# Kernel optimization log

Hardware: AMD Instinct MI355X
Metric: run time of the kernel (lower is better)

## Reference

```python
import jax, jax.numpy as jnp
import numpy as np

B, H, L, V = 128, 1024, 60, 50257


def setup_inputs() -> dict:
    key = jax.random.key(0)
    ks = jax.random.split(key, 14)
    s = 0.02
    f32 = jnp.float32
    return {
        "input": jax.random.randint(ks[0], (B,), 0, V),
        "hidden": jax.random.normal(ks[1], (1, B, H), f32),
        "encoder_outputs": jax.random.normal(ks[2], (B, L, H), f32),
        # learned parameters
        "emb": (jax.random.normal(ks[3], (V, H), f32) * s),
        "attn_W": (jax.random.normal(ks[4], (L, 2 * H), f32) * s),
        "attn_b": jnp.zeros((L,), f32),
        "comb_W": (jax.random.normal(ks[5], (H, 2 * H), f32) * s),
        "comb_b": jnp.zeros((H,), f32),
        "W_ih": (jax.random.normal(ks[6], (3 * H, H), f32) * s),
        "W_hh": (jax.random.normal(ks[7], (3 * H, H), f32) * s),
        "b_ih": jnp.zeros((3 * H,), f32),
        "b_hh": jnp.zeros((3 * H,), f32),
        "out_W": (jax.random.normal(ks[8], (V, H), f32) * s),
        "out_b": jnp.zeros((V,), f32),
    }


def reference(input, hidden, encoder_outputs, emb, attn_W, attn_b,
              comb_W, comb_b, W_ih, W_hh, b_ih, b_hh, out_W, out_b):
    # embedding lookup (dropout is identity in eval mode)
    embedded = emb[input]                      # [B, H]
    h = hidden[0]                              # [B, H]

    # Bahdanau-style attention over fixed max_length positions
    attn_logits = jnp.concatenate([embedded, h], axis=1) @ attn_W.T + attn_b  # [B, L]
    attn_weights = jax.nn.softmax(attn_logits, axis=1)                        # [B, L]
    attn_applied = jnp.einsum('bl,blh->bh', attn_weights, encoder_outputs)    # [B, H]

    # combine + relu
    x = jnp.concatenate([embedded, attn_applied], axis=1) @ comb_W.T + comb_b  # [B, H]
    x = jax.nn.relu(x)

    # single GRU step (PyTorch gate order: r, z, n)
    gi = x @ W_ih.T + b_ih                     # [B, 3H]
    gh = h @ W_hh.T + b_hh                     # [B, 3H]
    i_r, i_z, i_n = jnp.split(gi, 3, axis=1)
    h_r, h_z, h_n = jnp.split(gh, 3, axis=1)
    r = jax.nn.sigmoid(i_r + h_r)
    z = jax.nn.sigmoid(i_z + h_z)
    n = jnp.tanh(i_n + r * h_n)
    h_new = (1.0 - z) * n + z * h              # [B, H]

    # output projection + log_softmax over vocab
    logp = jax.nn.log_softmax(h_new @ out_W.T + out_b, axis=1)  # [B, V]
    return logp, h_new[None], attn_weights
```

## Files before the change

### kernel.cpp

```cpp
#include <hip/hip_runtime.h>
#include <hip/hip_bf16.h>

#define B_ 128
#define H_ 1024
#define L_ 60
#define V_ 50257

typedef __attribute__((ext_vector_type(8))) short bf16x8;
typedef __attribute__((ext_vector_type(4))) short bf16x4;
typedef __attribute__((ext_vector_type(4))) float f32x4;

__device__ __forceinline__ unsigned short f2bf(float f) {
  union { __hip_bfloat16 h; unsigned short u; } v;
  v.h = __float2bfloat16(f);
  return v.u;
}

__device__ __forceinline__ void gl_lds16(const void* g, void* l) {
  __builtin_amdgcn_global_load_lds(
      (const __attribute__((address_space(1))) unsigned int*)g,
      (__attribute__((address_space(3))) unsigned int*)l, 16, 0, 0);
}

#define SBAR()   __builtin_amdgcn_s_barrier()
#define SCHED0() __builtin_amdgcn_sched_barrier(0)
__device__ __forceinline__ void lwait0() { asm volatile("s_waitcnt lgkmcnt(0)" ::: "memory"); }
__device__ __forceinline__ void vwait4() { asm volatile("s_waitcnt vmcnt(4)" ::: "memory"); }
__device__ __forceinline__ void vwait0() { asm volatile("s_waitcnt vmcnt(0)" ::: "memory"); }

__device__ __forceinline__ size_t packIdx(int b, int k) {
  int s = k >> 5;
  int bm = b >> 4;
  int lane = (b & 15) | (((k >> 3) & 3) << 4);
  return ((size_t)((s * 8 + bm) * 64 + lane) << 3) | (size_t)(k & 7);
}

__global__ __launch_bounds__(256) void k_front(
    const int* __restrict__ input, const float* __restrict__ hidden,
    const float* __restrict__ emb, const float* __restrict__ attn_W,
    const float* __restrict__ attn_b, unsigned short* __restrict__ aXa,
    unsigned short* __restrict__ aH, float* __restrict__ lbuf)
{
  int bx = blockIdx.x;
  if (bx < 512) {
    int idx = bx * 256 + threadIdx.x;
    int b = idx >> 10, j = idx & (H_ - 1);
    float e = emb[(size_t)input[b] * H_ + j];
    float h = hidden[idx];
    size_t p = packIdx(b, j);
    aXa[p] = f2bf(e);
    aH[p]  = f2bf(h);
  } else {
    int t = threadIdx.x, wv = t >> 6, lane = t & 63;
    int task = (bx - 512) * 4 + wv;
    int b = task / L_, l = task - b * L_;
    const float* erow = emb + (size_t)input[b] * H_;
    const float* hrow = hidden + (size_t)b * H_;
    const float* wr = attn_W + (size_t)l * (2 * H_);
    float acc = 0.f;
    #pragma unroll 4
    for (int i = 0; i < 16; ++i) {
      int m = lane + i * 64;
      acc += erow[m] * wr[m] + hrow[m] * wr[H_ + m];
    }
    #pragma unroll
    for (int off = 32; off; off >>= 1) acc += __shfl_xor(acc, off);
    if (lane == 0) lbuf[b * 64 + l] = acc + attn_b[l];
  }
}

__global__ __launch_bounds__(256) void k_appsm(
    const float* __restrict__ enc, const float* __restrict__ lbuf,
    float* __restrict__ attnw, unsigned short* __restrict__ aXa)
{
  __shared__ float sWt[64];
  int b = blockIdx.x, q = blockIdx.y, t = threadIdx.x;
  if (t < 64) {
    float v = (t < L_) ? lbuf[b * 64 + t] : -1e30f;
    float m = v;
    #pragma unroll
    for (int off = 32; off; off >>= 1) m = fmaxf(m, __shfl_xor(m, off));
    float e = (t < L_) ? __expf(v - m) : 0.f;
    float s = e;
    #pragma unroll
    for (int off = 32; off; off >>= 1) s += __shfl_xor(s, off);
    float w = e / s;
    sWt[t] = w;
    if (q == 0 && t < L_) attnw[b * L_ + t] = w;
  }
  __syncthreads();
  int col = q * 256 + t;
  const float* eb = enc + (size_t)b * L_ * H_ + col;
  float acc = 0.f;
  #pragma unroll 4
  for (int l = 0; l < L_; ++l) acc += sWt[l] * eb[(size_t)l * H_];
  aXa[packIdx(b, H_ + col)] = f2bf(acc);
}

__global__ __launch_bounds__(256, 6) void k_gemm(
    const unsigned short* __restrict__ Apk, const unsigned short* __restrict__ Apk2,
    const float* __restrict__ Wt, const float* __restrict__ Wt2,
    const float* __restrict__ bias, float* __restrict__ Cdir,
    float* __restrict__ Cpart, float* __restrict__ Cpart2,
    float* __restrict__ pms, int K, int N, int nchunks, int halfY, int nblkx)
{
  __shared__ __align__(16) unsigned short bufW[2][32 * 32];
  __shared__ __align__(16) unsigned short bufA[2][8 * 512];
  int t = threadIdx.x, wv = t >> 6, lane = t & 63;
  int y = blockIdx.y;
  const unsigned short* A = Apk;
  const float* W = Wt;
  float* CP = Cpart;
  int sidx = y;
  if (halfY && y >= halfY) { A = Apk2; W = Wt2; CP = Cpart2; sidx = y - halfY; }
  int chunk0 = sidx * nchunks;
  int cend = chunk0 + nchunks;
  int n0 = blockIdx.x * 32;
  int ch = wv & 1;
  int bm0 = (wv >> 1) * 4;
  int g = lane >> 4;

  int tr = t >> 3, tq = t & 7;
  int wgcol = n0 + tr; if (wgcol >= N) wgcol = N - 1;
  const float* wsrc = W + (size_t)wgcol * K + tq * 4;
  int wsl = ((tq >> 1) ^ ((tr >> 1) & 3)) * 8 + (tq & 1) * 4;
  unsigned short* wd0 = &bufW[0][tr * 32 + wsl];
  unsigned short* wd1 = &bufW[1][tr * 32 + wsl];

  f32x4 acc[4];
  #pragma unroll
  for (int i = 0; i < 4; ++i) acc[i] = (f32x4){0.f, 0.f, 0.f, 0.f};

  auto GWl = [&](int kc) { return *(const float4*)(wsrc + (size_t)kc * 32); };
  auto WST = [&](unsigned short* d, float4 w) {
    bf16x4 v;
    v[0] = (short)f2bf(w.x); v[1] = (short)f2bf(w.y);
    v[2] = (short)f2bf(w.z); v[3] = (short)f2bf(w.w);
    *(bf16x4*)d = v;
  };
  auto GA = [&](int kc, unsigned short* bA) {
    #pragma unroll
    for (int f2 = 0; f2 < 2; ++f2) {
      int f = wv * 2 + f2;
      const unsigned short* src = A + ((size_t)kc * 8 + f) * 512 + lane * 8;
      gl_lds16(src, bA + f * 512);
    }
  };
  auto COMP = [&](const unsigned short* bW, const unsigned short* bA) {
    int rr = ch * 16 + (lane & 15);
    int sp = g ^ ((rr >> 1) & 3);
    bf16x8 bfr = *(const bf16x8*)&bW[rr * 32 + sp * 8];
    #pragma unroll
    for (int bm = 0; bm < 4; ++bm) {
      bf16x8 af = *(const bf16x8*)&bA[(bm0 + bm) * 512 + lane * 8];
      acc[bm] = __builtin_amdgcn_mfma_f32_16x16x32_bf16(af, bfr, acc[bm], 0, 0, 0);
    }
  };

  float4 wreg[4];
  wreg[0] = GWl(chunk0);
  wreg[1] = GWl(chunk0 + 1);
  SCHED0();
  GA(chunk0, bufA[0]);
  GA(chunk0 + 1, bufA[1]);
  SCHED0();
  wreg[2] = GWl(chunk0 + 2);
  wreg[3] = GWl(chunk0 + 3);
  SCHED0();
  WST(wd0, wreg[0]);
  WST(wd1, wreg[1]);
  lwait0(); vwait4(); SCHED0(); SBAR();

  int c = chunk0;
  for (; c + 8 <= cend; c += 4) {
    #pragma unroll
    for (int hh = 0; hh < 4; ++hh) {
      COMP(bufW[hh & 1], bufA[hh & 1]);
      SCHED0(); SBAR(); SCHED0();
      GA(c + hh + 2, bufA[hh & 1]);
      SCHED0();
      wreg[hh] = GWl(c + hh + 4);
      SCHED0();
      WST((hh & 1) ? wd1 : wd0, wreg[(hh + 2) & 3]);
      lwait0(); vwait4(); SCHED0(); SBAR();
    }
  }

  {
    COMP(bufW[0], bufA[0]);
    SCHED0(); SBAR(); SCHED0();
    GA(c + 2, bufA[0]);
    WST(wd0, wreg[2]);
    lwait0(); vwait0(); SCHED0(); SBAR();
    COMP(bufW[1], bufA[1]);
    SCHED0(); SBAR(); SCHED0();
    GA(c + 3, bufA[1]);
    WST(wd1, wreg[3]);
    lwait0(); vwait0(); SCHED0(); SBAR();
    COMP(bufW[0], bufA[0]);
    COMP(bufW[1], bufA[1]);
  }

  int col = n0 + ch * 16 + (lane & 15);
  float bv = (bias && col < N) ? bias[col] : 0.f;
  int rb = (lane >> 4) * 4;
  if (CP) {
    float* dst = CP + (size_t)sidx * B_ * N;
    #pragma unroll
    for (int bm = 0; bm < 4; ++bm)
      #pragma unroll
      for (int r = 0; r < 4; ++r) {
        int row = (bm0 + bm) * 16 + rb + r;
        if (col < N) dst[(size_t)row * N + col] = acc[bm][r];
      }
  } else {
    #pragma unroll
    for (int bm = 0; bm < 4; ++bm)
      #pragma unroll
      for (int r = 0; r < 4; ++r) {
        int row = (bm0 + bm) * 16 + rb + r;
        if (col < N) Cdir[(size_t)row * N + col] = acc[bm][r] + bv;
      }
    if (pms) {
      #pragma unroll
      for (int bm = 0; bm < 4; ++bm)
        #pragma unroll
        for (int r = 0; r < 4; ++r) {
          int row = (bm0 + bm) * 16 + rb + r;
          float m = (col < N) ? (acc[bm][r] + bv) : -1e30f;
          #pragma unroll
          for (int off = 8; off; off >>= 1) m = fmaxf(m, __shfl_xor(m, off));
          float e = (col < N) ? __expf(acc[bm][r] + bv - m) : 0.f;
          #pragma unroll
          for (int off = 8; off; off >>= 1) e += __shfl_xor(e, off);
          if ((lane & 15) == 0) {
            size_t o = ((size_t)row * (2 * nblkx) + blockIdx.x * 2 + ch) * 2;
            pms[o] = m; pms[o + 1] = e;
          }
        }
    }
  }
}

__global__ __launch_bounds__(256) void k_reduce_comb(
    const float* __restrict__ parts, const float* __restrict__ bias,
    unsigned short* __restrict__ aX)
{
  int idx = blockIdx.x * 256 + threadIdx.x;
  int b = idx >> 10, j = idx & (H_ - 1);
  float s = bias[j];
  #pragma unroll
  for (int p = 0; p < 16; ++p) s += parts[(size_t)p * B_ * H_ + idx];
  s = fmaxf(s, 0.f);
  aX[packIdx(b, j)] = f2bf(s);
}

__global__ __launch_bounds__(256) void k_gate(
    const float* __restrict__ giP, const float* __restrict__ ghP,
    const float* __restrict__ b_ih, const float* __restrict__ b_hh,
    const float* __restrict__ hidden, float* __restrict__ hnew,
    unsigned short* __restrict__ aHn)
{
  int idx = blockIdx.x * 256 + threadIdx.x;
  int b = idx >> 10, j = idx & (H_ - 1);
  size_t base = (size_t)b * 3 * H_;
  float ir = b_ih[j], iz = b_ih[H_ + j], in_ = b_ih[2 * H_ + j];
  float hr = b_hh[j], hz = b_hh[H_ + j], hn = b_hh[2 * H_ + j];
  #pragma unroll
  for (int p = 0; p < 4; ++p) {
    const float* gi = giP + (size_t)p * B_ * 3 * H_ + base;
    const float* gh = ghP + (size_t)p * B_ * 3 * H_ + base;
    ir += gi[j]; iz += gi[H_ + j]; in_ += gi[2 * H_ + j];
    hr += gh[j]; hz += gh[H_ + j]; hn += gh[2 * H_ + j];
  }
  float r = 1.f / (1.f + __expf(-(ir + hr)));
  float z = 1.f / (1.f + __expf(-(iz + hz)));
  float n = tanhf(in_ + r * hn);
  float h = hidden[idx];
  float hv = (1.f - z) * n + z * h;
  hnew[idx] = hv;
  aHn[packIdx(b, j)] = f2bf(hv);
}

#define SL_ 6283
__global__ __launch_bounds__(256) void k_lsub(
    float* __restrict__ logits, const float* __restrict__ pms, int nblk2)
{
  __shared__ float sm[4], ss[4], sc;
  int b = blockIdx.x, sl = blockIdx.y, t = threadIdx.x;
  float M = -1e30f, S = 0.f;
  for (int i = t; i < nblk2; i += 256) {
    float m = pms[((size_t)b * nblk2 + i) * 2];
    float s = pms[((size_t)b * nblk2 + i) * 2 + 1];
    float nm = fmaxf(M, m);
    S = S * __expf(M - nm) + s * __expf(m - nm);
    M = nm;
  }
  #pragma unroll
  for (int off = 32; off; off >>= 1) {
    float m2 = __shfl_xor(M, off), s2 = __shfl_xor(S, off);
    float nm = fmaxf(M, m2);
    S = S * __expf(M - nm) + s2 * __expf(m2 - nm);
    M = nm;
  }
  if ((t & 63) == 0) { sm[t >> 6] = M; ss[t >> 6] = S; }
  __syncthreads();
  if (t == 0) {
    float Mf = sm[0], Sf = ss[0];
    #pragma unroll
    for (int i = 1; i < 4; ++i) {
      float nm = fmaxf(Mf, sm[i]);
      Sf = Sf * __expf(Mf - nm) + ss[i] * __expf(sm[i] - nm);
      Mf = nm;
    }
    sc = Mf + logf(Sf);
  }
  __syncthreads();
  float c = sc;
  int v0 = sl * SL_;
  int v1 = v0 + SL_; if (v1 > V_) v1 = V_;
  float* row = logits + (size_t)b * V_;
  for (int v = v0 + t; v < v1; v += 256) row[v] -= c;
}

extern "C" void kernel_launch(void* const* d_in, const int* in_sizes, int n_in,
                              void* d_out, int out_size, void* d_ws, size_t ws_size,
                              hipStream_t stream)
{
  const int*   input  = (const int*)d_in[0];
  const float* hidden = (const float*)d_in[1];
  const float* enc    = (const float*)d_in[2];
  const float* emb    = (const float*)d_in[3];
  const float* attn_W = (const float*)d_in[4];
  const float* attn_b = (const float*)d_in[5];
  const float* comb_W = (const float*)d_in[6];
  const float* comb_b = (const float*)d_in[7];
  const float* W_ih   = (const float*)d_in[8];
  const float* W_hh   = (const float*)d_in[9];
  const float* b_ih   = (const float*)d_in[10];
  const float* b_hh   = (const float*)d_in[11];
  const float* out_W  = (const float*)d_in[12];
  const float* out_b  = (const float*)d_in[13];

  float* out    = (float*)d_out;
  float* logits = out;
  float* hnew   = out + (size_t)B_ * V_;
  float* attnw  = hnew + (size_t)B_ * H_;

  const int NBLK = (V_ + 31) / 32;
  char* ws = (char*)d_ws;
  unsigned short* aXa = (unsigned short*)(ws);
  unsigned short* aH  = (unsigned short*)(ws + 524288);
  unsigned short* aX  = (unsigned short*)(ws + 786432);
  unsigned short* aHn = (unsigned short*)(ws + 1048576);
  float* lbuf  = (float*)(ws + 1310720);
  float* combP = (float*)(ws + 4194304);
  float* giP   = (float*)(ws + 4194304);
  float* ghP   = (float*)(ws + 4194304 + 6291456);
  float* pms   = (float*)(ws + 20971520);

  k_front<<<512 + (B_ * L_) / 4, 256, 0, stream>>>(input, hidden, emb, attn_W, attn_b,
                                                   aXa, aH, lbuf);
  k_appsm<<<dim3(B_, 4), 256, 0, stream>>>(enc, lbuf, attnw, aXa);
  k_gemm<<<dim3(32, 16), 256, 0, stream>>>(aXa, nullptr, comb_W, nullptr, nullptr,
                                           nullptr, combP, nullptr, nullptr,
                                           2 * H_, H_, 4, 0, 0);
  k_reduce_comb<<<(B_ * H_) / 256, 256, 0, stream>>>(combP, comb_b, aX);
  k_gemm<<<dim3(96, 8), 256, 0, stream>>>(aX, aH, W_ih, W_hh, nullptr,
                                          nullptr, giP, ghP, nullptr,
                                          H_, 3 * H_, 8, 4, 0);
  k_gate<<<(B_ * H_) / 256, 256, 0, stream>>>(giP, ghP, b_ih, b_hh, hidden, hnew, aHn);
  k_gemm<<<dim3(NBLK, 1), 256, 0, stream>>>(aHn, nullptr, out_W, nullptr, out_b,
                                            logits, nullptr, nullptr, pms,
                                            H_, V_, 32, 0, NBLK);
  k_lsub<<<dim3(B_, 8), 256, 0, stream>>>(logits, pms, 2 * NBLK);
}
```

Measured before the change: 146.0 us.

## Drop LDS staging in GEMM; load operands directly and shuffle weights via bpermute

The GEMM kernel no longer stages weight and activation tiles through double-buffered shared memory with barriers and explicit waitcnt pipelining. Each wave now loads its own fp32 weight slice, converts it to bf16, and redistributes it into the MFMA B-fragment layout with ds_bpermute. Activation fragments are read straight from global memory in the pre-packed layout. This removes barriers and LDS traffic, at the cost of redundant global reads of A across waves and reliance on the compiler to hide load latency instead of the hand-written prefetch pipeline.

Result: slower. 177.3 us (+21.5%).

```diff
diff --git a/kernel.cpp b/kernel.cpp
--- a/kernel.cpp
+++ b/kernel.cpp
@@ -7,7 +7,6 @@
 #define V_ 50257
 
 typedef __attribute__((ext_vector_type(8))) short bf16x8;
-typedef __attribute__((ext_vector_type(4))) short bf16x4;
 typedef __attribute__((ext_vector_type(4))) float f32x4;
 
 __device__ __forceinline__ unsigned short f2bf(float f) {
@@ -15,18 +14,6 @@
   v.h = __float2bfloat16(f);
   return v.u;
 }
-
-__device__ __forceinline__ void gl_lds16(const void* g, void* l) {
-  __builtin_amdgcn_global_load_lds(
-      (const __attribute__((address_space(1))) unsigned int*)g,
-      (__attribute__((address_space(3))) unsigned int*)l, 16, 0, 0);
-}
-
-#define SBAR()   __builtin_amdgcn_s_barrier()
-#define SCHED0() __builtin_amdgcn_sched_barrier(0)
-__device__ __forceinline__ void lwait0() { asm volatile("s_waitcnt lgkmcnt(0)" ::: "memory"); }
-__device__ __forceinline__ void vwait4() { asm volatile("s_waitcnt vmcnt(4)" ::: "memory"); }
-__device__ __forceinline__ void vwait0() { asm volatile("s_waitcnt vmcnt(0)" ::: "memory"); }
 
 __device__ __forceinline__ size_t packIdx(int b, int k) {
   int s = k >> 5;
@@ -104,8 +91,6 @@
     float* __restrict__ Cpart, float* __restrict__ Cpart2,
     float* __restrict__ pms, int K, int N, int nchunks, int halfY, int nblkx)
 {
-  __shared__ __align__(16) unsigned short bufW[2][32 * 32];
-  __shared__ __align__(16) unsigned short bufA[2][8 * 512];
   int t = threadIdx.x, wv = t >> 6, lane = t & 63;
   int y = blockIdx.y;
   const unsigned short* A = Apk;
@@ -118,87 +103,39 @@
   int n0 = blockIdx.x * 32;
   int ch = wv & 1;
   int bm0 = (wv >> 1) * 4;
-  int g = lane >> 4;
-
-  int tr = t >> 3, tq = t & 7;
-  int wgcol = n0 + tr; if (wgcol >= N) wgcol = N - 1;
-  const float* wsrc = W + (size_t)wgcol * K + tq * 4;
-  int wsl = ((tq >> 1) ^ ((tr >> 1) & 3)) * 8 + (tq & 1) * 4;
-  unsigned short* wd0 = &bufW[0][tr * 32 + wsl];
-  unsigned short* wd1 = &bufW[1][tr * 32 + wsl];
+
+  int wrow = n0 + ch * 16 + (lane >> 2);
+  if (wrow >= N) wrow = N - 1;
+  const float* wsrc = W + (size_t)wrow * K + (lane & 3) * 8;
+  int bidx = (4 * (lane & 15) + (lane >> 4)) * 4;
 
   f32x4 acc[4];
   #pragma unroll
   for (int i = 0; i < 4; ++i) acc[i] = (f32x4){0.f, 0.f, 0.f, 0.f};
 
-  auto GWl = [&](int kc) { return *(const float4*)(wsrc + (size_t)kc * 32); };
-  auto WST = [&](unsigned short* d, float4 w) {
-    bf16x4 v;
-    v[0] = (short)f2bf(w.x); v[1] = (short)f2bf(w.y);
-    v[2] = (short)f2bf(w.z); v[3] = (short)f2bf(w.w);
-    *(bf16x4*)d = v;
-  };
-  auto GA = [&](int kc, unsigned short* bA) {
-    #pragma unroll
-    for (int f2 = 0; f2 < 2; ++f2) {
-      int f = wv * 2 + f2;
-      const unsigned short* src = A + ((size_t)kc * 8 + f) * 512 + lane * 8;
-      gl_lds16(src, bA + f * 512);
-    }
-  };
-  auto COMP = [&](const unsigned short* bW, const unsigned short* bA) {
-    int rr = ch * 16 + (lane & 15);
-    int sp = g ^ ((rr >> 1) & 3);
-    bf16x8 bfr = *(const bf16x8*)&bW[rr * 32 + sp * 8];
-    #pragma unroll
-    for (int bm = 0; bm < 4; ++bm) {
-      bf16x8 af = *(const bf16x8*)&bA[(bm0 + bm) * 512 + lane * 8];
-      acc[bm] = __builtin_amdgcn_mfma_f32_16x16x32_bf16(af, bfr, acc[bm], 0, 0, 0);
-    }
-  };
-
-  float4 wreg[4];
-  wreg[0] = GWl(chunk0);
-  wreg[1] = GWl(chunk0 + 1);
-  SCHED0();
-  GA(chunk0, bufA[0]);
-  GA(chunk0 + 1, bufA[1]);
-  SCHED0();
-  wreg[2] = GWl(chunk0 + 2);
-  wreg[3] = GWl(chunk0 + 3);
-  SCHED0();
-  WST(wd0, wreg[0]);
-  WST(wd1, wreg[1]);
-  lwait0(); vwait4(); SCHED0(); SBAR();
-
-  int c = chunk0;
-  for (; c + 8 <= cend; c += 4) {
-    #pragma unroll
-    for (int hh = 0; hh < 4; ++hh) {
-      COMP(bufW[hh & 1], bufA[hh & 1]);
-      SCHED0(); SBAR(); SCHED0();
-      GA(c + hh + 2, bufA[hh & 1]);
-      SCHED0();
-      wreg[hh] = GWl(c + hh + 4);
-      SCHED0();
-      WST((hh & 1) ? wd1 : wd0, wreg[(hh + 2) & 3]);
-      lwait0(); vwait4(); SCHED0(); SBAR();
-    }
-  }
-
-  {
-    COMP(bufW[0], bufA[0]);
-    SCHED0(); SBAR(); SCHED0();
-    GA(c + 2, bufA[0]);
-    WST(wd0, wreg[2]);
-    lwait0(); vwait0(); SCHED0(); SBAR();
-    COMP(bufW[1], bufA[1]);
-    SCHED0(); SBAR(); SCHED0();
-    GA(c + 3, bufA[1]);
-    WST(wd1, wreg[3]);
-    lwait0(); vwait0(); SCHED0(); SBAR();
-    COMP(bufW[0], bufA[0]);
-    COMP(bufW[1], bufA[1]);
+  const bf16x8* apg = (const bf16x8*)A;
+
+  #pragma unroll 4
+  for (int c = chunk0; c < cend; ++c) {
+    const float* p = wsrc + (size_t)c * 32;
+    float4 wlo = *(const float4*)p;
+    float4 whi = *(const float4*)(p + 4);
+    bf16x8 af[4];
+    #pragma unroll
+    for (int bm = 0; bm < 4; ++bm)
+      af[bm] = apg[((size_t)c * 8 + bm0 + bm) * 64 + lane];
+    unsigned q0 = (unsigned)f2bf(wlo.x) | ((unsigned)f2bf(wlo.y) << 16);
+    unsigned q1 = (unsigned)f2bf(wlo.z) | ((unsigned)f2bf(wlo.w) << 16);
+    unsigned q2 = (unsigned)f2bf(whi.x) | ((unsigned)f2bf(whi.y) << 16);
+    unsigned q3 = (unsigned)f2bf(whi.z) | ((unsigned)f2bf(whi.w) << 16);
+    union { bf16x8 v; unsigned u[4]; } bw;
+    bw.u[0] = __builtin_amdgcn_ds_bpermute(bidx, (int)q0);
+    bw.u[1] = __builtin_amdgcn_ds_bpermute(bidx, (int)q1);
+    bw.u[2] = __builtin_amdgcn_ds_bpermute(bidx, (int)q2);
+    bw.u[3] = __builtin_amdgcn_ds_bpermute(bidx, (int)q3);
+    #pragma unroll
+    for (int bm = 0; bm < 4; ++bm)
+      acc[bm] = __builtin_amdgcn_mfma_f32_16x16x32_bf16(af[bm], bw.v, acc[bm], 0, 0, 0);
   }
 
   int col = n0 + ch * 16 + (lane & 15);
```
